# Performance work log

Hardware: AMD Instinct MI355X
Metric: run time of the kernel (lower is better)

## Reference

```python
import jax, jax.numpy as jnp
import numpy as np

EMBED = 3072
NQ = 32
NKV = 8
HD = EMBED // NQ  # 96
GROUPS = NQ // NKV  # 4
ROPE_BASE = 10000.0


def apply_rope(t, positions):
    # t: [b, h, s, d]; positions: [s] int
    d = t.shape[-1]
    inv_freq = 1.0 / (ROPE_BASE ** (jnp.arange(0, d, 2, dtype=jnp.float32) / d))  # [d/2]
    ang = positions.astype(jnp.float32)[:, None] * inv_freq[None, :]  # [s, d/2]
    cos = jnp.cos(ang)[None, None]  # [1,1,s,d/2]
    sin = jnp.sin(ang)[None, None]
    t1, t2 = t[..., : d // 2], t[..., d // 2 :]
    return jnp.concatenate([t1 * cos - t2 * sin, t2 * cos + t1 * sin], axis=-1)


def setup_inputs() -> dict:
    key = jax.random.key(0)
    k1, k2, k3 = jax.random.split(key, 3)
    b, s = 2, 2048
    x = jax.random.normal(k1, (b, s, EMBED), dtype=jnp.float32)
    positions = jnp.arange(s, dtype=jnp.int32)
    mask = jnp.triu(jnp.ones((s, s), dtype=bool), k=1)  # True = masked (causal)
    qkv_size = NQ * HD + 2 * NKV * HD  # 4608
    W_qkv = jax.random.normal(k2, (qkv_size, EMBED), dtype=jnp.float32) * (EMBED ** -0.5)
    W_o = jax.random.normal(k3, (EMBED, EMBED), dtype=jnp.float32) * (EMBED ** -0.5)
    return {"x": x, "positions": positions, "mask": mask, "W_qkv": W_qkv, "W_o": W_o}


def reference(x, positions, mask, W_qkv, W_o):
    b, s, _ = x.shape
    scaling = HD ** -0.5
    qkv = x @ W_qkv.T  # [b, s, 4608]
    q_size, kv_size = NQ * HD, NKV * HD
    q = qkv[..., :q_size].reshape(b, s, NQ, HD).transpose(0, 2, 1, 3)          # [b,NQ,s,d]
    k = qkv[..., q_size : q_size + kv_size].reshape(b, s, NKV, HD).transpose(0, 2, 1, 3)
    v = qkv[..., q_size + kv_size :].reshape(b, s, NKV, HD).transpose(0, 2, 1, 3)
    q = apply_rope(q, positions)
    k = apply_rope(k, positions)
    q = q.reshape(b, NKV, GROUPS, s, HD)
    scores = jnp.einsum("bkgsd,bktd->bkgst", q, k) * scaling  # [b,NKV,G,s,s]
    scores = jnp.where(mask[None, None, None], -jnp.inf, scores)
    attn = jax.nn.softmax(scores, axis=-1)
    out = jnp.einsum("bkgst,bktd->bkgsd", attn, v)
    out = out.reshape(b, NQ, s, HD).transpose(0, 2, 1, 3).reshape(b, s, NQ * HD)
    return out @ W_o.T
```

## Files before the change

kernel.cpp:

```cpp
#include <hip/hip_runtime.h>
#include <cstdint>

typedef unsigned short u16;
typedef unsigned int u32;
typedef __attribute__((ext_vector_type(4))) float f32x4;
typedef __attribute__((ext_vector_type(8))) __bf16 bf16x8;
typedef __attribute__((ext_vector_type(8))) unsigned short u16x8;
typedef __attribute__((ext_vector_type(4))) unsigned int u32x4;

#define S_LEN 2048
#define BATCH 2
#define NQH 32
#define NKVH 8
#define HD 96
#define EMB 3072
#define QKVN 4608
#define KOFF 3072
#define VOFF 3840

__device__ __forceinline__ u16 f2b(float f) {
    u32 u = __float_as_uint(f);
    u32 r = (u + 0x7fffu + ((u >> 16) & 1u)) >> 16;
    return (u16)r;
}
__device__ __forceinline__ float b2f(u16 h) { return __uint_as_float(((u32)h) << 16); }
__device__ __forceinline__ u32 cvtpk(float lo, float hi) {
    u32 r;
    asm("v_cvt_pk_bf16_f32 %0, %1, %2" : "=v"(r) : "v"(lo), "v"(hi));
    return r;
}

__global__ __launch_bounds__(256) void conv_f2b(const float* __restrict__ in,
                                                u16* __restrict__ outp, int n8) {
    const int i = blockIdx.x * 256 + threadIdx.x;
    if (i >= n8) return;
    const f32x4* q = (const f32x4*)(in + (size_t)i * 8);
    const f32x4 a = q[0], b = q[1];
    u16x8 t;
#pragma unroll
    for (int j = 0; j < 4; ++j) {
        t[j] = f2b(a[j]);
        t[j + 4] = f2b(b[j]);
    }
    *(u16x8*)(outp + (size_t)i * 8) = t;
}

typedef __attribute__((address_space(1))) const uint32_t gas_u32;
typedef __attribute__((address_space(3))) uint32_t las_u32;
__device__ __forceinline__ void gld_lds16(const u16* g, u16* l) {
    __builtin_amdgcn_global_load_lds((gas_u32*)g, (las_u32*)l, 16, 0, 0);
}

#define WAITV4 asm volatile("s_waitcnt vmcnt(4)" ::: "memory")
#define WAITV0 asm volatile("s_waitcnt vmcnt(0)" ::: "memory")
#define BARRIER __builtin_amdgcn_s_barrier()
#define SCHEDB __builtin_amdgcn_sched_barrier(0)

template <bool OUTF32>
__global__ __launch_bounds__(256, 2) void gemm_bt_p(const u16* __restrict__ Ap,
                                                    const u16* __restrict__ Bp,
                                                    void* __restrict__ Cp,
                                                    int M, int N, int K, int ldc) {
    __shared__ __align__(16) u16 S[2 * 16384];
    const int tid = threadIdx.x;
    const int wave = tid >> 6, lane = tid & 63;
    const int lrow = lane & 15, lhi = lane >> 4;
    const int bm = blockIdx.y * 128, bn = blockIdx.x * 128;
    const int wm = (wave >> 1) * 64, wn = (wave & 1) * 64;
    const int xsl = ((lhi ^ (lrow & 3) ^ ((lrow >> 2) & 3)) << 3);
    const int srow = tid >> 2;
    const int scol = (((tid & 3) ^ ((tid >> 2) & 3) ^ ((tid >> 4) & 3))) * 8;
    const u16* gA0 = Ap + (size_t)(bm + srow) * K + scol;
    const u16* gA1 = Ap + (size_t)(bm + 64 + srow) * K + scol;
    const u16* gB0 = Bp + (size_t)(bn + srow) * K + scol;
    const u16* gB1 = Bp + (size_t)(bn + 64 + srow) * K + scol;
    u16* const dbase = S + (tid & 192) * 8;

    f32x4 acc[4][4] = {};
    const int nt = K >> 6;

    gld_lds16(gA0, dbase);
    gld_lds16(gA1, dbase + 2048);
    gld_lds16(gB0, dbase + 8192);
    gld_lds16(gB1, dbase + 8192 + 2048);
    gld_lds16(gA0 + 32, dbase + 4096);
    gld_lds16(gA1 + 32, dbase + 4096 + 2048);
    gld_lds16(gB0 + 32, dbase + 8192 + 4096);
    gld_lds16(gB1 + 32, dbase + 8192 + 4096 + 2048);

    for (int t = 0; t + 1 < nt; ++t) {
        const int cur = t & 1;
        const u16* Ab = S + cur * 16384;
        const u16* Bb = Ab + 8192;
        u16* dn = dbase + (cur ^ 1) * 16384;
        const int ko = (t + 1) << 6;

        WAITV4;
        BARRIER;
        SCHEDB;
        gld_lds16(gA0 + ko, dn);
        gld_lds16(gA1 + ko, dn + 2048);
        bf16x8 af[4], bf0[2], bf1[2];
#pragma unroll
        for (int mi = 0; mi < 4; ++mi)
            af[mi] = *(const bf16x8*)(Ab + (wm + mi * 16 + lrow) * 32 + xsl);
#pragma unroll
        for (int ni = 0; ni < 2; ++ni)
            bf0[ni] = *(const bf16x8*)(Bb + (wn + ni * 16 + lrow) * 32 + xsl);
        __builtin_amdgcn_s_setprio(1);
#pragma unroll
        for (int mi = 0; mi < 4; ++mi)
#pragma unroll
            for (int ni = 0; ni < 2; ++ni)
                acc[mi][ni] = __builtin_amdgcn_mfma_f32_16x16x32_bf16(af[mi], bf0[ni],
                                                                      acc[mi][ni], 0, 0, 0);
        __builtin_amdgcn_s_setprio(0);
        gld_lds16(gB0 + ko, dn + 8192);
        gld_lds16(gB1 + ko, dn + 8192 + 2048);
#pragma unroll
        for (int ni = 0; ni < 2; ++ni)
            bf1[ni] = *(const bf16x8*)(Bb + (wn + (ni + 2) * 16 + lrow) * 32 + xsl);
        __builtin_amdgcn_s_setprio(1);
#pragma unroll
        for (int mi = 0; mi < 4; ++mi)
#pragma unroll
            for (int ni = 0; ni < 2; ++ni)
                acc[mi][ni + 2] = __builtin_amdgcn_mfma_f32_16x16x32_bf16(af[mi], bf1[ni],
                                                                          acc[mi][ni + 2], 0, 0, 0);
        __builtin_amdgcn_s_setprio(0);

        WAITV4;
        BARRIER;
        SCHEDB;
        gld_lds16(gA0 + ko + 32, dn + 4096);
        gld_lds16(gA1 + ko + 32, dn + 4096 + 2048);
#pragma unroll
        for (int mi = 0; mi < 4; ++mi)
            af[mi] = *(const bf16x8*)(Ab + 4096 + (wm + mi * 16 + lrow) * 32 + xsl);
#pragma unroll
        for (int ni = 0; ni < 2; ++ni)
            bf0[ni] = *(const bf16x8*)(Bb + 4096 + (wn + ni * 16 + lrow) * 32 + xsl);
        __builtin_amdgcn_s_setprio(1);
#pragma unroll
        for (int mi = 0; mi < 4; ++mi)
#pragma unroll
            for (int ni = 0; ni < 2; ++ni)
                acc[mi][ni] = __builtin_amdgcn_mfma_f32_16x16x32_bf16(af[mi], bf0[ni],
                                                                      acc[mi][ni], 0, 0, 0);
        __builtin_amdgcn_s_setprio(0);
        gld_lds16(gB0 + ko + 32, dn + 8192 + 4096);
        gld_lds16(gB1 + ko + 32, dn + 8192 + 4096 + 2048);
#pragma unroll
        for (int ni = 0; ni < 2; ++ni)
            bf1[ni] = *(const bf16x8*)(Bb + 4096 + (wn + (ni + 2) * 16 + lrow) * 32 + xsl);
        __builtin_amdgcn_s_setprio(1);
#pragma unroll
        for (int mi = 0; mi < 4; ++mi)
#pragma unroll
            for (int ni = 0; ni < 2; ++ni)
                acc[mi][ni + 2] = __builtin_amdgcn_mfma_f32_16x16x32_bf16(af[mi], bf1[ni],
                                                                          acc[mi][ni + 2], 0, 0, 0);
        __builtin_amdgcn_s_setprio(0);
    }

    {
        const int cur = (nt - 1) & 1;
        const u16* Ab = S + cur * 16384;
        const u16* Bb = Ab + 8192;
        WAITV4;
        BARRIER;
        SCHEDB;
        bf16x8 af[4], bfr[4];
#pragma unroll
        for (int mi = 0; mi < 4; ++mi)
            af[mi] = *(const bf16x8*)(Ab + (wm + mi * 16 + lrow) * 32 + xsl);
#pragma unroll
        for (int ni = 0; ni < 4; ++ni)
            bfr[ni] = *(const bf16x8*)(Bb + (wn + ni * 16 + lrow) * 32 + xsl);
#pragma unroll
        for (int mi = 0; mi < 4; ++mi)
#pragma unroll
            for (int ni = 0; ni < 4; ++ni)
                acc[mi][ni] = __builtin_amdgcn_mfma_f32_16x16x32_bf16(af[mi], bfr[ni],
                                                                      acc[mi][ni], 0, 0, 0);
        WAITV0;
        BARRIER;
        SCHEDB;
#pragma unroll
        for (int mi = 0; mi < 4; ++mi)
            af[mi] = *(const bf16x8*)(Ab + 4096 + (wm + mi * 16 + lrow) * 32 + xsl);
#pragma unroll
        for (int ni = 0; ni < 4; ++ni)
            bfr[ni] = *(const bf16x8*)(Bb + 4096 + (wn + ni * 16 + lrow) * 32 + xsl);
#pragma unroll
        for (int mi = 0; mi < 4; ++mi)
#pragma unroll
            for (int ni = 0; ni < 4; ++ni)
                acc[mi][ni] = __builtin_amdgcn_mfma_f32_16x16x32_bf16(af[mi], bfr[ni],
                                                                      acc[mi][ni], 0, 0, 0);
    }

    const int orow = bm + wm + lhi * 4;
    const int ocol = bn + wn + lrow;
#pragma unroll
    for (int mi = 0; mi < 4; ++mi)
#pragma unroll
        for (int ni = 0; ni < 4; ++ni)
#pragma unroll
            for (int r = 0; r < 4; ++r) {
                const size_t idx = (size_t)(orow + mi * 16 + r) * ldc + ocol + ni * 16;
                if constexpr (OUTF32)
                    ((float*)Cp)[idx] = acc[mi][ni][r];
                else
                    ((u16*)Cp)[idx] = f2b(acc[mi][ni][r]);
            }
}

__global__ __launch_bounds__(256) void gqa_rope(u16* __restrict__ qkv,
                                                const int* __restrict__ positions) {
    int i = blockIdx.x * 256 + threadIdx.x;
    const int pair = i % 48;
    int t = i / 48;
    const int head = t % (NQH + NKVH);
    const int bs = t / (NQH + NKVH);
    const int pos = positions[bs & (S_LEN - 1)];
    const size_t base = (size_t)bs * QKVN + (head < NQH ? head * HD : KOFF + (head - NQH) * HD);
    const float invf = __expf(-(float)(2 * pair) * (1.0f / 96.0f) * 9.210340371976184f);
    const float ang = (float)pos * invf;
    float sn, cs;
    __sincosf(ang, &sn, &cs);
    const float t1 = b2f(qkv[base + pair]);
    const float t2 = b2f(qkv[base + 48 + pair]);
    qkv[base + pair] = f2b(t1 * cs - t2 * sn);
    qkv[base + 48 + pair] = f2b(t2 * cs + t1 * sn);
}

__global__ __launch_bounds__(256) void gqa_attn3(const u16* __restrict__ qkv,
                                                 u16* __restrict__ out) {
    __shared__ __align__(16) u16 Ks[64 * 96];
    __shared__ __align__(16) u16 Vt[96 * 72];

    const int tid = threadIdx.x;
    const int wave = tid >> 6, lane = tid & 63;
    const int lrow = lane & 15, lhi = lane >> 4;
    const int bx = blockIdx.x;
    const int qt32 = 63 - (bx >> 4);
    const int kvh = (bx >> 1) & 7, bb = bx & 1;
    const int qh = kvh * 4 + wave;
    const int srow0 = bb * S_LEN + qt32 * 32;
    const int kb_last = (qt32 * 32 + 31) >> 6;
    const float cl2 = 0.10206207261596575f * 1.4426950408889634f;

    bf16x8 bq[2][3];
#pragma unroll
    for (int qt = 0; qt < 2; ++qt)
#pragma unroll
        for (int kd = 0; kd < 3; ++kd)
            bq[qt][kd] = *(const bf16x8*)(qkv + (size_t)(srow0 + qt * 16 + lrow) * QKVN +
                                          qh * 96 + kd * 32 + lhi * 8);

    float m_s[2] = {-3e38f, -3e38f}, l_s[2] = {0.0f, 0.0f};
    f32x4 oacc[6][2] = {};

    const int s0 = lrow + ((lane & 16) ? 32 : 0);
    const int s1 = s0 + 16;
    const bool khi = (lane & 32) != 0;

    const size_t kvrow0 = (size_t)(bb * S_LEN) * QKVN;
    for (int kb = 0; kb <= kb_last; ++kb) {
        __syncthreads();
        const size_t kbase = kvrow0 + (size_t)(kb * 64) * QKVN + KOFF + kvh * 96;
        const size_t vbase = kvrow0 + (size_t)(kb * 64) * QKVN + VOFF + kvh * 96;
        for (int u = tid; u < 768; u += 256) {
            const int oct = u % 12, row = u / 12;
            *(u16x8*)(Ks + row * 96 + oct * 8) =
                *(const u16x8*)(qkv + kbase + (size_t)row * QKVN + oct * 8);
        }
        for (int u = tid; u < 768; u += 256) {
            const int d = u % 96, so8 = u / 96;
            u16x8 v8;
#pragma unroll
            for (int j = 0; j < 8; ++j) v8[j] = qkv[vbase + (size_t)(so8 * 8 + j) * QKVN + d];
            *(u16x8*)(Vt + d * 72 + so8 * 8) = v8;
        }
        __syncthreads();

        bf16x8 ka[4][3];
#pragma unroll
        for (int kt = 0; kt < 4; ++kt)
#pragma unroll
            for (int kd = 0; kd < 3; ++kd)
                ka[kt][kd] = *(const bf16x8*)(Ks + (kt * 16 + lrow) * 96 + kd * 32 + lhi * 8);

        const int qoff = qt32 * 32 - kb * 64;
        const bool lastkb = (kb == kb_last);
        u32 bp[2][2][4];

#pragma unroll
        for (int qt = 0; qt < 2; ++qt) {
            const int qrelmax = qoff + qt * 16 + 15;
            f32x4 sacc[4] = {};
#pragma unroll
            for (int kt = 0; kt < 4; ++kt) {
                if (lastkb && kt * 16 > qrelmax) continue;
#pragma unroll
                for (int kd = 0; kd < 3; ++kd)
                    sacc[kt] = __builtin_amdgcn_mfma_f32_16x16x32_bf16(ka[kt][kd], bq[qt][kd],
                                                                       sacc[kt], 0, 0, 0);
            }
            float p[4][4];
            float mx = -3e38f;
            if (lastkb) {
                const int qrel = qoff + qt * 16 + lrow;
#pragma unroll
                for (int kt = 0; kt < 4; ++kt)
#pragma unroll
                    for (int r = 0; r < 4; ++r) {
                        const bool live = (kt * 16 + lhi * 4 + r) <= qrel;
                        const float s = live ? sacc[kt][r] : -3e38f;
                        p[kt][r] = s;
                        mx = fmaxf(mx, s);
                    }
            } else {
#pragma unroll
                for (int kt = 0; kt < 4; ++kt)
#pragma unroll
                    for (int r = 0; r < 4; ++r) {
                        p[kt][r] = sacc[kt][r];
                        mx = fmaxf(mx, sacc[kt][r]);
                    }
            }
            mx = fmaxf(mx, __shfl_xor(mx, 16));
            mx = fmaxf(mx, __shfl_xor(mx, 32));
            float mn = m_s[qt];
            if (!__all(mx - mn <= 20.0f)) {
                const float mnew = fmaxf(mn, mx);
                const float alpha = exp2f((mn - mnew) * cl2);
                m_s[qt] = mnew;
                mn = mnew;
                l_s[qt] *= alpha;
#pragma unroll
                for (int dt = 0; dt < 6; ++dt)
#pragma unroll
                    for (int r = 0; r < 4; ++r) oacc[dt][qt][r] *= alpha;
            }
            float rs = 0.0f;
#pragma unroll
            for (int kt = 0; kt < 4; ++kt)
#pragma unroll
                for (int r = 0; r < 4; ++r) {
                    const float pv = exp2f((p[kt][r] - mn) * cl2);
                    p[kt][r] = pv;
                    rs += pv;
                }
            rs += __shfl_xor(rs, 16);
            rs += __shfl_xor(rs, 32);
            l_s[qt] += rs;
            u32 pk[4][2];
#pragma unroll
            for (int kt = 0; kt < 4; ++kt) {
                pk[kt][0] = cvtpk(p[kt][0], p[kt][1]);
                pk[kt][1] = cvtpk(p[kt][2], p[kt][3]);
            }
#pragma unroll
            for (int kk = 0; kk < 2; ++kk) {
                const u32 a0 = (u32)__shfl((int)pk[kk * 2][0], s0, 64);
                const u32 b0 = (u32)__shfl((int)pk[kk * 2 + 1][0], s0, 64);
                const u32 a1 = (u32)__shfl((int)pk[kk * 2][1], s0, 64);
                const u32 b1 = (u32)__shfl((int)pk[kk * 2 + 1][1], s0, 64);
                const u32 a2 = (u32)__shfl((int)pk[kk * 2][0], s1, 64);
                const u32 b2 = (u32)__shfl((int)pk[kk * 2 + 1][0], s1, 64);
                const u32 a3 = (u32)__shfl((int)pk[kk * 2][1], s1, 64);
                const u32 b3 = (u32)__shfl((int)pk[kk * 2 + 1][1], s1, 64);
                bp[qt][kk][0] = khi ? b0 : a0;
                bp[qt][kk][1] = khi ? b1 : a1;
                bp[qt][kk][2] = khi ? b2 : a2;
                bp[qt][kk][3] = khi ? b3 : a3;
            }
        }

#pragma unroll
        for (int dt = 0; dt < 6; ++dt) {
            bf16x8 va[2];
#pragma unroll
            for (int kk = 0; kk < 2; ++kk)
                va[kk] = *(const bf16x8*)(Vt + (dt * 16 + lrow) * 72 + kk * 32 + lhi * 8);
#pragma unroll
            for (int qt = 0; qt < 2; ++qt)
#pragma unroll
                for (int kk = 0; kk < 2; ++kk) {
                    const u32x4 bv = {bp[qt][kk][0], bp[qt][kk][1], bp[qt][kk][2], bp[qt][kk][3]};
                    oacc[dt][qt] = __builtin_amdgcn_mfma_f32_16x16x32_bf16(
                        va[kk], __builtin_bit_cast(bf16x8, bv), oacc[dt][qt], 0, 0, 0);
                }
        }
    }

    const size_t obase = (size_t)srow0 * EMB + qh * 96;
#pragma unroll
    for (int qt = 0; qt < 2; ++qt) {
        const float inv = 1.0f / l_s[qt];
        const size_t rbase = obase + (size_t)(qt * 16 + lrow) * EMB;
#pragma unroll
        for (int dt = 0; dt < 6; ++dt)
#pragma unroll
            for (int rp = 0; rp < 2; ++rp) {
                const u32 pair = cvtpk(oacc[dt][qt][2 * rp] * inv, oacc[dt][qt][2 * rp + 1] * inv);
                *(u32*)(out + rbase + dt * 16 + lhi * 4 + 2 * rp) = pair;
            }
    }
}

extern "C" void kernel_launch(void* const* d_in, const int* in_sizes, int n_in,
                              void* d_out, int out_size, void* d_ws, size_t ws_size,
                              hipStream_t stream) {
    const float* x = (const float*)d_in[0];
    const int* positions = (const int*)d_in[1];
    const float* W_qkv = (const float*)d_in[3];
    const float* W_o = (const float*)d_in[4];
    float* out = (float*)d_out;

    const int M = BATCH * S_LEN;
    const size_t QKV_E = (size_t)M * QKVN;
    const size_t ATT_E = (size_t)M * EMB;
    const size_t X_E = (size_t)M * EMB;
    const size_t WQKV_E = (size_t)QKVN * EMB;
    const size_t WO_E = (size_t)EMB * EMB;

    u16* qkv = (u16*)d_ws;
    u16* scratch = qkv + QKV_E;
    u16* xb = scratch;
    u16* wqkvb = (u16*)d_out;
    u16* wob = (u16*)d_ws;

    conv_f2b<<<(int)(X_E / 8 / 256), 256, 0, stream>>>(x, xb, (int)(X_E / 8));
    conv_f2b<<<(int)(WQKV_E / 8 / 256), 256, 0, stream>>>(W_qkv, wqkvb, (int)(WQKV_E / 8));
    gemm_bt_p<false>
        <<<dim3(QKVN / 128, M / 128), 256, 0, stream>>>(xb, wqkvb, qkv, M, QKVN, EMB, QKVN);
    gqa_rope<<<(BATCH * S_LEN * (NQH + NKVH) * 48) / 256, 256, 0, stream>>>(qkv, positions);
    gqa_attn3<<<dim3(1024), 256, 0, stream>>>(qkv, scratch);
    conv_f2b<<<(int)(WO_E / 8 / 256), 256, 0, stream>>>(W_o, wob, (int)(WO_E / 8));
    gemm_bt_p<true>
        <<<dim3(EMB / 128, M / 128), 256, 0, stream>>>(scratch, wob, out, M, EMB, EMB, EMB);
}
```

Before: 612.1 us.

## Prefetch next K/V tile into registers, transpose V via LDS, remap GEMM blocks

The attention kernel now loads the next K/V block into registers while the current block is computed, so global latency overlaps with MFMA work. V is staged row-wise in LDS and transposed there, replacing strided scalar global loads. K rows are padded to reduce bank conflicts. The GEMM block index is remapped across 8 groups, presumably to spread neighbouring tiles across XCDs for cache locality. In exchange the kernel uses more registers and LDS and adds extra barriers.

```diff
diff --git a/kernel.cpp b/kernel.cpp
--- a/kernel.cpp
+++ b/kernel.cpp
@@ -17,6 +17,7 @@
 #define QKVN 4608
 #define KOFF 3072
 #define VOFF 3840
+#define KSP 104
 
 __device__ __forceinline__ u16 f2b(float f) {
     u32 u = __float_as_uint(f);
@@ -65,7 +66,19 @@
     const int tid = threadIdx.x;
     const int wave = tid >> 6, lane = tid & 63;
     const int lrow = lane & 15, lhi = lane >> 4;
-    const int bm = blockIdx.y * 128, bn = blockIdx.x * 128;
+
+    int bxi = blockIdx.x, byi = blockIdx.y;
+    {
+        const int gx = gridDim.x;
+        const int nwg = gx * gridDim.y;
+        if ((nwg & 7) == 0) {
+            int fid = byi * gx + bxi;
+            fid = (fid & 7) * (nwg >> 3) + (fid >> 3);
+            bxi = fid % gx;
+            byi = fid / gx;
+        }
+    }
+    const int bm = byi * 128, bn = bxi * 128;
     const int wm = (wave >> 1) * 64, wn = (wave & 1) * 64;
     const int xsl = ((lhi ^ (lrow & 3) ^ ((lrow >> 2) & 3)) << 3);
     const int srow = tid >> 2;
@@ -235,9 +248,10 @@
     qkv[base + 48 + pair] = f2b(t2 * cs + t1 * sn);
 }
 
-__global__ __launch_bounds__(256) void gqa_attn3(const u16* __restrict__ qkv,
+__global__ __launch_bounds__(256) void gqa_attn5(const u16* __restrict__ qkv,
                                                  u16* __restrict__ out) {
-    __shared__ __align__(16) u16 Ks[64 * 96];
+    __shared__ __align__(16) u16 Ks[64 * KSP];
+    __shared__ __align__(16) u16 Vtmp[64 * 96];
     __shared__ __align__(16) u16 Vt[96 * 72];
 
     const int tid = threadIdx.x;
@@ -267,30 +281,57 @@
     const bool khi = (lane & 32) != 0;
 
     const size_t kvrow0 = (size_t)(bb * S_LEN) * QKVN;
+    u16x8 kreg[3], vreg[3];
+
+    {
+        const size_t kbase = kvrow0 + KOFF + (size_t)kvh * 96;
+        const size_t vbase = kvrow0 + VOFF + (size_t)kvh * 96;
+#pragma unroll
+        for (int i = 0; i < 3; ++i) {
+            const int u = tid + 256 * i;
+            const int so = (u % 12) * 8, sr = u / 12;
+            kreg[i] = *(const u16x8*)(qkv + kbase + (size_t)sr * QKVN + so);
+            vreg[i] = *(const u16x8*)(qkv + vbase + (size_t)sr * QKVN + so);
+        }
+#pragma unroll
+        for (int i = 0; i < 3; ++i) {
+            const int u = tid + 256 * i;
+            const int so = (u % 12) * 8, sr = u / 12;
+            *(u16x8*)(Ks + sr * KSP + so) = kreg[i];
+            *(u16x8*)(Vtmp + sr * 96 + so) = vreg[i];
+        }
+        __syncthreads();
+#pragma unroll
+        for (int i = 0; i < 3; ++i) {
+            const int u = tid + 256 * i;
+            const int td = u % 96, ts8 = u / 96;
+            u16x8 c;
+#pragma unroll
+            for (int j = 0; j < 8; ++j) c[j] = Vtmp[(ts8 * 8 + j) * 96 + td];
+            *(u16x8*)(Vt + td * 72 + ts8 * 8) = c;
+        }
+    }
+
     for (int kb = 0; kb <= kb_last; ++kb) {
+        if (kb < kb_last) {
+            const size_t kbase2 = kvrow0 + (size_t)((kb + 1) * 64) * QKVN + KOFF + kvh * 96;
+            const size_t vbase2 = kvrow0 + (size_t)((kb + 1) * 64) * QKVN + VOFF + kvh * 96;
+#pragma unroll
+            for (int i = 0; i < 3; ++i) {
+                const int u = tid + 256 * i;
+                const int so = (u % 12) * 8, sr = u / 12;
+                kreg[i] = *(const u16x8*)(qkv + kbase2 + (size_t)sr * QKVN + so);
+                vreg[i] = *(const u16x8*)(qkv + vbase2 + (size_t)sr * QKVN + so);
+            }
+        }
         __syncthreads();
-        const size_t kbase = kvrow0 + (size_t)(kb * 64) * QKVN + KOFF + kvh * 96;
-        const size_t vbase = kvrow0 + (size_t)(kb * 64) * QKVN + VOFF + kvh * 96;
-        for (int u = tid; u < 768; u += 256) {
-            const int oct = u % 12, row = u / 12;
-            *(u16x8*)(Ks + row * 96 + oct * 8) =
-                *(const u16x8*)(qkv + kbase + (size_t)row * QKVN + oct * 8);
-        }
-        for (int u = tid; u < 768; u += 256) {
-            const int d = u % 96, so8 = u / 96;
-            u16x8 v8;
-#pragma unroll
-            for (int j = 0; j < 8; ++j) v8[j] = qkv[vbase + (size_t)(so8 * 8 + j) * QKVN + d];
-            *(u16x8*)(Vt + d * 72 + so8 * 8) = v8;
-        }
-        __syncthreads();
 
         bf16x8 ka[4][3];
 #pragma unroll
         for (int kt = 0; kt < 4; ++kt)
 #pragma unroll
             for (int kd = 0; kd < 3; ++kd)
-                ka[kt][kd] = *(const bf16x8*)(Ks + (kt * 16 + lrow) * 96 + kd * 32 + lhi * 8);
+                ka[kt][kd] = *(const bf16x8*)(Ks + (kt * 16 + lrow) * KSP + kd * 32 + lhi * 8);
 
         const int qoff = qt32 * 32 - kb * 64;
         const bool lastkb = (kb == kb_last);
@@ -394,6 +435,27 @@
                         va[kk], __builtin_bit_cast(bf16x8, bv), oacc[dt][qt], 0, 0, 0);
                 }
         }
+
+        __syncthreads();
+        if (kb < kb_last) {
+#pragma unroll
+            for (int i = 0; i < 3; ++i) {
+                const int u = tid + 256 * i;
+                const int so = (u % 12) * 8, sr = u / 12;
+                *(u16x8*)(Ks + sr * KSP + so) = kreg[i];
+                *(u16x8*)(Vtmp + sr * 96 + so) = vreg[i];
+            }
+            __syncthreads();
+#pragma unroll
+            for (int i = 0; i < 3; ++i) {
+                const int u = tid + 256 * i;
+                const int td = u % 96, ts8 = u / 96;
+                u16x8 c;
+#pragma unroll
+                for (int j = 0; j < 8; ++j) c[j] = Vtmp[(ts8 * 8 + j) * 96 + td];
+                *(u16x8*)(Vt + td * 72 + ts8 * 8) = c;
+            }
+        }
     }
 
     const size_t obase = (size_t)srow0 * EMB + qh * 96;
@@ -438,7 +500,7 @@
     gemm_bt_p<false>
         <<<dim3(QKVN / 128, M / 128), 256, 0, stream>>>(xb, wqkvb, qkv, M, QKVN, EMB, QKVN);
     gqa_rope<<<(BATCH * S_LEN * (NQH + NKVH) * 48) / 256, 256, 0, stream>>>(qkv, positions);
-    gqa_attn3<<<dim3(1024), 256, 0, stream>>>(qkv, scratch);
+    gqa_attn5<<<dim3(1024), 256, 0, stream>>>(qkv, scratch);
     conv_f2b<<<(int)(WO_E / 8 / 256), 256, 0, stream>>>(W_o, wob, (int)(WO_E / 8));
     gemm_bt_p<true>
         <<<dim3(EMB / 128, M / 128), 256, 0, stream>>>(scratch, wob, out, M, EMB, EMB, EMB);
```

New measurement: 618.2 us. No clear change (+1.0%).
